# Performance work log

Hardware: AMD Instinct MI355X
Metric: run time of the kernel (lower is better)

Reference implementation:

```python
import jax, jax.numpy as jnp
import numpy as np

N = 50000
E = 800000
IN_C, HID_C, OUT_C = 256, 128, 64


def setup_inputs() -> dict:
    key = jax.random.key(0)
    k1, k2, k3, k4 = jax.random.split(key, 4)
    x = jax.random.normal(k1, (N, IN_C), dtype=jnp.float32)
    edge_index = jax.random.randint(k2, (2, E), 0, N, dtype=jnp.int64)
    # Glorot-ish init for GCN weights, zero bias (PyG default)
    W1 = jax.random.normal(k3, (IN_C, HID_C), dtype=jnp.float32) / np.sqrt(IN_C)
    b1 = jnp.zeros((HID_C,), dtype=jnp.float32)
    W2 = jax.random.normal(k4, (HID_C, OUT_C), dtype=jnp.float32) / np.sqrt(HID_C)
    b2 = jnp.zeros((OUT_C,), dtype=jnp.float32)
    return {"x": x, "edge_index": edge_index, "W1": W1, "b1": b1, "W2": W2, "b2": b2}


def _gcn_norm(edge_index, num_nodes):
    # Add self-loops, compute symmetric normalization D^-1/2 A D^-1/2 (PyG GCNConv default)
    loops = jnp.arange(num_nodes, dtype=edge_index.dtype)
    src = jnp.concatenate([edge_index[0], loops])  # message sources
    dst = jnp.concatenate([edge_index[1], loops])  # aggregation targets
    deg = jax.ops.segment_sum(jnp.ones_like(dst, dtype=jnp.float32), dst,
                              num_segments=num_nodes)
    dinv = jnp.where(deg > 0, jax.lax.rsqrt(deg), 0.0)
    norm = dinv[src] * dinv[dst]  # [E+N]
    return src, dst, norm


def _gcn_conv(x, W, b, src, dst, norm, num_nodes):
    h = x @ W                                   # [N, out]
    msg = h[src] * norm[:, None]                # gather + scale, [E+N, out]
    out = jax.ops.segment_sum(msg, dst, num_segments=num_nodes)  # scatter-add
    return out + b


def reference(x, edge_index, W1, b1, W2, b2):
    num_nodes = x.shape[0]
    src, dst, norm = _gcn_norm(edge_index, num_nodes)
    h = _gcn_conv(x, W1, b1, src, dst, norm, num_nodes)
    h = jax.nn.relu(h)
    # F.dropout(training=False) -> identity at inference
    return _gcn_conv(h, W2, b2, src, dst, norm, num_nodes)
```

## Files before the change

### kernel.cpp

```cpp
#include <hip/hip_runtime.h>
#include <hip/hip_bf16.h>


typedef __attribute__((ext_vector_type(8))) short short8;
typedef __attribute__((ext_vector_type(4))) float f32x4;

union BF8 {
    short8 s;
    uint4 u;
    __hip_bfloat162 h[4];
};

__device__ __forceinline__ unsigned short f32_to_bf16_rne(float f) {
    unsigned u = __float_as_uint(f);
    return (unsigned short)((u + 0x7fffu + ((u >> 16) & 1u)) >> 16);
}
__device__ __forceinline__ float bf_lo(unsigned v) { return __uint_as_float(v << 16); }
__device__ __forceinline__ float bf_hi(unsigned v) { return __uint_as_float(v & 0xffff0000u); }

#define ACHUNK 2048
#define BSH 6
#define BN 64
#define CAP 2048
#define EPT (CAP / 256)

__global__ void wfrag_zero_kernel(const float* __restrict__ W1, const float* __restrict__ W2,
                                  unsigned short* __restrict__ w1f,
                                  unsigned short* __restrict__ w2f,
                                  int* __restrict__ counts, int* __restrict__ bcursor,
                                  int n, int nbk) {
    int i = blockIdx.x * blockDim.x + threadIdx.x;
    if (i < n) counts[i] = 0;
    if (i < nbk) bcursor[i] = 0;
    const float* W;
    unsigned short* WF;
    int KS, NCOL, idx;
    if (i < 32768) {
        W = W1; WF = w1f; KS = 8; NCOL = 128; idx = i;
    } else if (i < 32768 + 8192) {
        W = W2; WF = w2f; KS = 4; NCOL = 64; idx = i - 32768;
    } else return;
    int j = idx & 7;
    int lane = (idx >> 3) & 63;
    int f = idx >> 9;
    int ks = f % KS, nt = f / KS;
    int m16 = lane & 15, quad = lane >> 4;
    int ncol = nt * 16 + m16;
    int k = ks * 32 + quad * 8 + j;
    WF[idx] = f32_to_bf16_rne(W[k * NCOL + ncol]);
}

__global__ __launch_bounds__(256) void gemm1_bucket_kernel(
    const float* __restrict__ A, const unsigned short* __restrict__ BFRAG,
    unsigned short* __restrict__ C, int M, int gGemm,
    const int* __restrict__ src, const int* __restrict__ dst,
    int* __restrict__ counts, int* __restrict__ bcursor,
    int2* __restrict__ tmp, int e, int nbk) {
    constexpr int NT = 8, KS = 8;
    constexpr int K = KS * 32;
    constexpr int LSTRIDE = K + 8;
    __shared__ char smem[64 * LSTRIDE * 2];

    const int tid = threadIdx.x;
    if ((int)blockIdx.x < gGemm) {
        unsigned short* Alds = (unsigned short*)smem;
        const int wave = tid >> 6, lane = tid & 63;
        const int quad = lane >> 4, m16 = lane & 15;
        const int rowBase = blockIdx.x * 64;

        constexpr int HALVES = K / 128;
#pragma unroll
        for (int h = 0; h < HALVES; h++) {
            f32x4 v[8];
#pragma unroll
            for (int it = 0; it < 8; it++) {
                int p = (h * 8 + it) * 1024 + tid * 4;
                int rg = rowBase + p / K;
                if (rg >= M) rg = M - 1;
                v[it] = *(const f32x4*)(A + (size_t)rg * K + (p % K));
            }
#pragma unroll
            for (int it = 0; it < 8; it++) {
                int p = (h * 8 + it) * 1024 + tid * 4;
                BF8 cv;
                cv.h[0] = __float22bfloat162_rn(make_float2(v[it].x, v[it].y));
                cv.h[1] = __float22bfloat162_rn(make_float2(v[it].z, v[it].w));
                *(uint2*)&Alds[(p / K) * LSTRIDE + (p % K)] = make_uint2(cv.u.x, cv.u.y);
            }
        }
        __syncthreads();

        const unsigned short* Afrag0 = &Alds[(wave * 16 + m16) * LSTRIDE + quad * 8];
        const uint4* Bfrag = (const uint4*)BFRAG + lane;

        f32x4 acc[NT];
#pragma unroll
        for (int nt = 0; nt < NT; nt++) acc[nt] = f32x4{0.f, 0.f, 0.f, 0.f};
#pragma unroll
        for (int ks = 0; ks < KS; ks++) {
            BF8 af;
            af.u = *(const uint4*)(Afrag0 + ks * 32);
#pragma unroll
            for (int nt = 0; nt < NT; nt++) {
                BF8 bf;
                bf.u = Bfrag[(nt * KS + ks) * 64];
                acc[nt] = __builtin_amdgcn_mfma_f32_16x16x32_bf16(af.s, bf.s, acc[nt], 0, 0, 0);
            }
        }
        const int rowOut = rowBase + wave * 16 + quad * 4;
#pragma unroll
        for (int nt = 0; nt < NT; nt++) {
#pragma unroll
            for (int r = 0; r < 4; r++) {
                int row = rowOut + r;
                if (row < M)
                    C[(size_t)row * 128 + nt * 16 + m16] = f32_to_bf16_rne(acc[nt][r]);
            }
        }
    } else {
        int* sdst = (int*)smem;
        int* hist = (int*)(smem + ACHUNK * 4);
        const int b0 = blockIdx.x - gGemm;
        const int start = b0 * ACHUNK;
        const int cnt = min(ACHUNK, e - start);
        for (int t = tid; t < nbk; t += 256) hist[t] = 0;
        __syncthreads();
        for (int i = tid; i < cnt; i += 256) {
            int d = dst[start + i];
            sdst[i] = d;
            atomicAdd(&counts[d], 1);
            atomicAdd(&hist[d >> BSH], 1);
        }
        __syncthreads();
        for (int t = tid; t < nbk; t += 256) {
            int h = hist[t];
            hist[t] = (h > 0) ? atomicAdd(&bcursor[t], h) : 0;
        }
        __syncthreads();
        for (int i = tid; i < cnt; i += 256) {
            int d = sdst[i];
            int slot = atomicAdd(&hist[d >> BSH], 1);
            if (slot < CAP)
                tmp[(size_t)(d >> BSH) * CAP + slot] = make_int2(src[start + i], d);
        }
    }
}

__global__ __launch_bounds__(256) void aggsort_gemm2_kernel(
    const int* __restrict__ counts, const int2* __restrict__ tmp,
    const int* __restrict__ bcursor,
    const unsigned short* __restrict__ hb,
    const float* __restrict__ bias1,
    const unsigned short* __restrict__ w2frag,
    int2* __restrict__ sedge, int2* __restrict__ nodeRange,
    unsigned short* __restrict__ h2, int n) {
    constexpr int LSTRIDE = 136;
    __shared__ int ecnt[BN];
    __shared__ int estart[BN];
    __shared__ int lcur[BN];
    __shared__ float ndinv[BN];
    __shared__ int ssrc[CAP];
    __shared__ float swt[CAP];
    __shared__ unsigned short a1lds[BN * LSTRIDE];

    const int tid = threadIdx.x;
    const int b = blockIdx.x;
    const int nodeBase = b << BSH;
    const int nNodes = min(BN, n - nodeBase);
    const int cnt = min(bcursor[b], CAP);

    if (tid < BN) ecnt[tid] = 0;
    __syncthreads();

    int2 er[EPT];
#pragma unroll
    for (int j = 0; j < EPT; j++) {
        int i = tid + j * 256;
        if (i < cnt) {
            int2 r = tmp[(size_t)b * CAP + i];
            er[j] = r;
            atomicAdd(&ecnt[r.y - nodeBase], 1);
        } else {
            er[j].x = -1;
            er[j].y = 0;
        }
    }
    __syncthreads();

    if (tid < BN) {
        int c = ecnt[tid];
        int x = c;
#pragma unroll
        for (int off = 1; off < 64; off <<= 1) {
            int y = __shfl_up(x, off, 64);
            if (tid >= off) x += y;
        }
        int st = x - c;
        estart[tid] = st;
        lcur[tid] = st;
        ndinv[tid] = (tid < nNodes) ? rsqrtf((float)counts[nodeBase + tid] + 1.0f) : 0.0f;
        if (tid < nNodes) nodeRange[nodeBase + tid] = make_int2(b * CAP + st, c);
    }
    __syncthreads();

#pragma unroll
    for (int j = 0; j < EPT; j++) {
        if (er[j].x >= 0) {
            int ln = er[j].y - nodeBase;
            float w = rsqrtf((float)counts[er[j].x] + 1.0f) * ndinv[ln];
            int pos = atomicAdd(&lcur[ln], 1);
            ssrc[pos] = er[j].x;
            swt[pos] = w;
            sedge[(size_t)b * CAP + pos] = make_int2(er[j].x, __float_as_int(w));
        }
    }
    __syncthreads();

    const int sub = tid & 15;
    const int qw = tid >> 4;
    for (int pass = 0; pass < BN / 16; pass++) {
        int ln = pass * 16 + qw;
        float a0 = 0.f, a1 = 0.f, a2 = 0.f, a3 = 0.f;
        float a4 = 0.f, a5 = 0.f, a6 = 0.f, a7 = 0.f;
        if (ln < nNodes) {
            int node = nodeBase + ln;
            float di = ndinv[ln];
            float d2 = di * di;
            uint4 sv = ((const uint4*)(hb + (size_t)node * 128))[sub];
            a0 = d2 * bf_lo(sv.x); a1 = d2 * bf_hi(sv.x);
            a2 = d2 * bf_lo(sv.y); a3 = d2 * bf_hi(sv.y);
            a4 = d2 * bf_lo(sv.z); a5 = d2 * bf_hi(sv.z);
            a6 = d2 * bf_lo(sv.w); a7 = d2 * bf_hi(sv.w);
            int beg = estart[ln];
            int end = beg + ecnt[ln];
            int i = beg;
            for (; i + 4 <= end; i += 4) {
                int s[4]; float w[4]; uint4 v[4];
#pragma unroll
                for (int j = 0; j < 4; j++) { s[j] = ssrc[i + j]; w[j] = swt[i + j]; }
#pragma unroll
                for (int j = 0; j < 4; j++)
                    v[j] = ((const uint4*)(hb + (size_t)s[j] * 128))[sub];
#pragma unroll
                for (int j = 0; j < 4; j++) {
                    a0 = fmaf(w[j], bf_lo(v[j].x), a0); a1 = fmaf(w[j], bf_hi(v[j].x), a1);
                    a2 = fmaf(w[j], bf_lo(v[j].y), a2); a3 = fmaf(w[j], bf_hi(v[j].y), a3);
                    a4 = fmaf(w[j], bf_lo(v[j].z), a4); a5 = fmaf(w[j], bf_hi(v[j].z), a5);
                    a6 = fmaf(w[j], bf_lo(v[j].w), a6); a7 = fmaf(w[j], bf_hi(v[j].w), a7);
                }
            }
            for (; i < end; ++i) {
                int s = ssrc[i];
                float w = swt[i];
                uint4 v = ((const uint4*)(hb + (size_t)s * 128))[sub];
                a0 = fmaf(w, bf_lo(v.x), a0); a1 = fmaf(w, bf_hi(v.x), a1);
                a2 = fmaf(w, bf_lo(v.y), a2); a3 = fmaf(w, bf_hi(v.y), a3);
                a4 = fmaf(w, bf_lo(v.z), a4); a5 = fmaf(w, bf_hi(v.z), a5);
                a6 = fmaf(w, bf_lo(v.w), a6); a7 = fmaf(w, bf_hi(v.w), a7);
            }
            float4 b0v = ((const float4*)bias1)[sub * 2];
            float4 b1v = ((const float4*)bias1)[sub * 2 + 1];
            a0 = fmaxf(a0 + b0v.x, 0.f); a1 = fmaxf(a1 + b0v.y, 0.f);
            a2 = fmaxf(a2 + b0v.z, 0.f); a3 = fmaxf(a3 + b0v.w, 0.f);
            a4 = fmaxf(a4 + b1v.x, 0.f); a5 = fmaxf(a5 + b1v.y, 0.f);
            a6 = fmaxf(a6 + b1v.z, 0.f); a7 = fmaxf(a7 + b1v.w, 0.f);
        }
        BF8 p;
        p.h[0] = __float22bfloat162_rn(make_float2(a0, a1));
        p.h[1] = __float22bfloat162_rn(make_float2(a2, a3));
        p.h[2] = __float22bfloat162_rn(make_float2(a4, a5));
        p.h[3] = __float22bfloat162_rn(make_float2(a6, a7));
        *(uint4*)&a1lds[ln * LSTRIDE + sub * 8] = p.u;
    }
    __syncthreads();

    const int wave = tid >> 6, lane = tid & 63;
    const int quad = lane >> 4, m16 = lane & 15;
    const unsigned short* Afrag0 = &a1lds[(wave * 16 + m16) * LSTRIDE + quad * 8];
    const uint4* Bfrag = (const uint4*)w2frag + lane;

    f32x4 acc[4];
#pragma unroll
    for (int nt = 0; nt < 4; nt++) acc[nt] = f32x4{0.f, 0.f, 0.f, 0.f};
#pragma unroll
    for (int ks = 0; ks < 4; ks++) {
        BF8 af;
        af.u = *(const uint4*)(Afrag0 + ks * 32);
#pragma unroll
        for (int nt = 0; nt < 4; nt++) {
            BF8 bf;
            bf.u = Bfrag[(nt * 4 + ks) * 64];
            acc[nt] = __builtin_amdgcn_mfma_f32_16x16x32_bf16(af.s, bf.s, acc[nt], 0, 0, 0);
        }
    }
    const int rowOut = wave * 16 + quad * 4;
#pragma unroll
    for (int nt = 0; nt < 4; nt++) {
#pragma unroll
        for (int r = 0; r < 4; r++) {
            int row = rowOut + r;
            if (row < nNodes)
                h2[(size_t)(nodeBase + row) * 64 + nt * 16 + m16] =
                    f32_to_bf16_rne(acc[nt][r]);
        }
    }
}

__global__ __launch_bounds__(256) void agg64_kernel(
    const int2* __restrict__ nodeRange, const int2* __restrict__ sedge,
    const unsigned short* __restrict__ hb, const int* __restrict__ counts,
    const float* __restrict__ bias, float* __restrict__ out, int n) {
    int node = blockIdx.x * 16 + (threadIdx.x >> 4);
    if (node >= n) return;
    int sub = threadIdx.x & 15;
    float di = rsqrtf((float)counts[node] + 1.0f);
    float d2 = di * di;
    uint2 sv = ((const uint2*)(hb + (size_t)node * 64))[sub];
    float a0 = d2 * bf_lo(sv.x), a1 = d2 * bf_hi(sv.x);
    float a2 = d2 * bf_lo(sv.y), a3 = d2 * bf_hi(sv.y);
    int2 nr = nodeRange[node];
    int beg = nr.x, end = nr.x + nr.y;
    int i = beg;
    for (; i + 8 <= end; i += 8) {
        int2 e[8];
        uint2 v[8];
#pragma unroll
        for (int j = 0; j < 8; j++) e[j] = sedge[i + j];
#pragma unroll
        for (int j = 0; j < 8; j++)
            v[j] = ((const uint2*)(hb + (size_t)e[j].x * 64))[sub];
#pragma unroll
        for (int j = 0; j < 8; j++) {
            float w = __int_as_float(e[j].y);
            a0 = fmaf(w, bf_lo(v[j].x), a0); a1 = fmaf(w, bf_hi(v[j].x), a1);
            a2 = fmaf(w, bf_lo(v[j].y), a2); a3 = fmaf(w, bf_hi(v[j].y), a3);
        }
    }
    for (; i + 4 <= end; i += 4) {
        int2 e[4];
        uint2 v[4];
#pragma unroll
        for (int j = 0; j < 4; j++) e[j] = sedge[i + j];
#pragma unroll
        for (int j = 0; j < 4; j++)
            v[j] = ((const uint2*)(hb + (size_t)e[j].x * 64))[sub];
#pragma unroll
        for (int j = 0; j < 4; j++) {
            float w = __int_as_float(e[j].y);
            a0 = fmaf(w, bf_lo(v[j].x), a0); a1 = fmaf(w, bf_hi(v[j].x), a1);
            a2 = fmaf(w, bf_lo(v[j].y), a2); a3 = fmaf(w, bf_hi(v[j].y), a3);
        }
    }
    for (; i < end; ++i) {
        int2 e = sedge[i];
        float w = __int_as_float(e.y);
        uint2 v = ((const uint2*)(hb + (size_t)e.x * 64))[sub];
        a0 = fmaf(w, bf_lo(v.x), a0); a1 = fmaf(w, bf_hi(v.x), a1);
        a2 = fmaf(w, bf_lo(v.y), a2); a3 = fmaf(w, bf_hi(v.y), a3);
    }
    float4 bv = ((const float4*)bias)[sub];
    ((float4*)(out + (size_t)node * 64))[sub] =
        make_float4(a0 + bv.x, a1 + bv.y, a2 + bv.z, a3 + bv.w);
}

extern "C" void kernel_launch(void* const* d_in, const int* in_sizes, int n_in,
                              void* d_out, int out_size, void* d_ws, size_t ws_size,
                              hipStream_t stream) {
    const float* x  = (const float*)d_in[0];
    const int*   ei = (const int*)d_in[1];
    const float* W1 = (const float*)d_in[2];
    const float* b1 = (const float*)d_in[3];
    const float* W2 = (const float*)d_in[4];
    const float* b2 = (const float*)d_in[5];
    float* out = (float*)d_out;

    const int IN_C = 256;
    const int N = in_sizes[0] / IN_C;
    const int E = in_sizes[1] / 2;
    const int* srcA = ei;
    const int* dstA = ei + E;

    char* ws = (char*)d_ws;
    const size_t KB = 1024, MB = 1024 * 1024;
    int*            counts    = (int*)(ws);
    int*            bcursor   = (int*)(ws + 256 * KB);
    unsigned short* w1f       = (unsigned short*)(ws + 1 * MB);
    unsigned short* w2f       = (unsigned short*)(ws + 1 * MB + 64 * KB);
    int2*           tmp       = (int2*)(ws + 2 * MB);
    int2*           sedge     = (int2*)(ws + 16 * MB);
    int2*           nodeRange = (int2*)(ws + 30 * MB);
    unsigned short* h1b       = (unsigned short*)(ws + 31 * MB);
    unsigned short* h2b       = (unsigned short*)(ws + 44 * MB);

    const int NB = (N + BN - 1) / BN;
    const int gGemm = (N + 63) / 64;
    const int nbA = (E + ACHUNK - 1) / ACHUNK;
    const int gWfrag = (max(N, 32768 + 8192) + 255) / 256;

    wfrag_zero_kernel<<<gWfrag, 256, 0, stream>>>(W1, W2, w1f, w2f, counts, bcursor, N, NB);
    gemm1_bucket_kernel<<<gGemm + nbA, 256, 0, stream>>>(
        x, w1f, h1b, N, gGemm, srcA, dstA, counts, bcursor, tmp, E, NB);
    aggsort_gemm2_kernel<<<NB, 256, 0, stream>>>(
        counts, tmp, bcursor, h1b, b1, w2f, sedge, nodeRange, h2b, N);
    agg64_kernel<<<(N + 15) / 16, 256, 0, stream>>>(nodeRange, sedge, h2b, counts, b2, out, N);
}
```

Before: 202.1 us.

## Shrink LDS footprints, add occupancy hints, and reorder bucket blocks first

The layer-1 GEMM now stages A in two K-halves of 128 columns, which halves its LDS tile, and the edge-bucketing blocks are scheduled before the GEMM blocks. The aggregation kernel drops its shared ssrc/swt staging and reads the sorted edge list from global memory. All three kernels get launch_bounds(256,8). Degree normalisation is computed from the local count instead of loading from the global counts array. Together these aim to raise occupancy and cut redundant loads, at the cost of an extra barrier in the GEMM and global re-reads of edges that likely hit cache.

```diff
diff --git a/kernel.cpp b/kernel.cpp
--- a/kernel.cpp
+++ b/kernel.cpp
@@ -50,61 +50,65 @@
     WF[idx] = f32_to_bf16_rne(W[k * NCOL + ncol]);
 }
 
-__global__ __launch_bounds__(256) void gemm1_bucket_kernel(
+__global__ __launch_bounds__(256, 8) void gemm1_bucket_kernel(
     const float* __restrict__ A, const unsigned short* __restrict__ BFRAG,
-    unsigned short* __restrict__ C, int M, int gGemm,
+    unsigned short* __restrict__ C, int M, int nbA,
     const int* __restrict__ src, const int* __restrict__ dst,
     int* __restrict__ counts, int* __restrict__ bcursor,
     int2* __restrict__ tmp, int e, int nbk) {
     constexpr int NT = 8, KS = 8;
     constexpr int K = KS * 32;
-    constexpr int LSTRIDE = K + 8;
-    __shared__ char smem[64 * LSTRIDE * 2];
+    constexpr int LSTRIDE = 136;
+    __shared__ unsigned short Alds[64 * LSTRIDE];
 
     const int tid = threadIdx.x;
-    if ((int)blockIdx.x < gGemm) {
-        unsigned short* Alds = (unsigned short*)smem;
+    if ((int)blockIdx.x >= nbA) {
         const int wave = tid >> 6, lane = tid & 63;
         const int quad = lane >> 4, m16 = lane & 15;
-        const int rowBase = blockIdx.x * 64;
-
-        constexpr int HALVES = K / 128;
-#pragma unroll
-        for (int h = 0; h < HALVES; h++) {
-            f32x4 v[8];
-#pragma unroll
-            for (int it = 0; it < 8; it++) {
-                int p = (h * 8 + it) * 1024 + tid * 4;
-                int rg = rowBase + p / K;
-                if (rg >= M) rg = M - 1;
-                v[it] = *(const f32x4*)(A + (size_t)rg * K + (p % K));
+        const int rowBase = (blockIdx.x - nbA) * 64;
+        const uint4* Bfrag = (const uint4*)BFRAG + lane;
+
+        f32x4 acc[NT];
+#pragma unroll
+        for (int nt = 0; nt < NT; nt++) acc[nt] = f32x4{0.f, 0.f, 0.f, 0.f};
+
+#pragma unroll
+        for (int h = 0; h < 2; h++) {
+            if (h) __syncthreads();
+#pragma unroll
+            for (int bt = 0; bt < 2; bt++) {
+                f32x4 v[4];
+#pragma unroll
+                for (int it = 0; it < 4; it++) {
+                    int p = (bt * 4 + it) * 1024 + tid * 4;
+                    int r = p >> 7, c = p & 127;
+                    int rg = rowBase + r;
+                    if (rg >= M) rg = M - 1;
+                    v[it] = *(const f32x4*)(A + (size_t)rg * K + h * 128 + c);
+                }
+#pragma unroll
+                for (int it = 0; it < 4; it++) {
+                    int p = (bt * 4 + it) * 1024 + tid * 4;
+                    int r = p >> 7, c = p & 127;
+                    BF8 cv;
+                    cv.h[0] = __float22bfloat162_rn(make_float2(v[it].x, v[it].y));
+                    cv.h[1] = __float22bfloat162_rn(make_float2(v[it].z, v[it].w));
+                    *(uint2*)&Alds[r * LSTRIDE + c] = make_uint2(cv.u.x, cv.u.y);
+                }
             }
-#pragma unroll
-            for (int it = 0; it < 8; it++) {
-                int p = (h * 8 + it) * 1024 + tid * 4;
-                BF8 cv;
-                cv.h[0] = __float22bfloat162_rn(make_float2(v[it].x, v[it].y));
-                cv.h[1] = __float22bfloat162_rn(make_float2(v[it].z, v[it].w));
-                *(uint2*)&Alds[(p / K) * LSTRIDE + (p % K)] = make_uint2(cv.u.x, cv.u.y);
-            }
-        }
-        __syncthreads();
-
-        const unsigned short* Afrag0 = &Alds[(wave * 16 + m16) * LSTRIDE + quad * 8];
-        const uint4* Bfrag = (const uint4*)BFRAG + lane;
-
-        f32x4 acc[NT];
-#pragma unroll
-        for (int nt = 0; nt < NT; nt++) acc[nt] = f32x4{0.f, 0.f, 0.f, 0.f};
-#pragma unroll
-        for (int ks = 0; ks < KS; ks++) {
-            BF8 af;
-            af.u = *(const uint4*)(Afrag0 + ks * 32);
-#pragma unroll
-            for (int nt = 0; nt < NT; nt++) {
-                BF8 bf;
-                bf.u = Bfrag[(nt * KS + ks) * 64];
-                acc[nt] = __builtin_amdgcn_mfma_f32_16x16x32_bf16(af.s, bf.s, acc[nt], 0, 0, 0);
+            __syncthreads();
+            const unsigned short* Afrag0 = &Alds[(wave * 16 + m16) * LSTRIDE + quad * 8];
+#pragma unroll
+            for (int ks = 0; ks < 4; ks++) {
+                BF8 af;
+                af.u = *(const uint4*)(Afrag0 + ks * 32);
+                int kg = h * 4 + ks;
+#pragma unroll
+                for (int nt = 0; nt < NT; nt++) {
+                    BF8 bf;
+                    bf.u = Bfrag[(nt * KS + kg) * 64];
+                    acc[nt] = __builtin_amdgcn_mfma_f32_16x16x32_bf16(af.s, bf.s, acc[nt], 0, 0, 0);
+                }
             }
         }
         const int rowOut = rowBase + wave * 16 + quad * 4;
@@ -118,9 +122,9 @@
             }
         }
     } else {
-        int* sdst = (int*)smem;
-        int* hist = (int*)(smem + ACHUNK * 4);
-        const int b0 = blockIdx.x - gGemm;
+        int* sdst = (int*)Alds;
+        int* hist = (int*)((char*)Alds + ACHUNK * 4);
+        const int b0 = blockIdx.x;
         const int start = b0 * ACHUNK;
         const int cnt = min(ACHUNK, e - start);
         for (int t = tid; t < nbk; t += 256) hist[t] = 0;
@@ -146,7 +150,7 @@
     }
 }
 
-__global__ __launch_bounds__(256) void aggsort_gemm2_kernel(
+__global__ __launch_bounds__(256, 8) void aggsort_gemm2_kernel(
     const int* __restrict__ counts, const int2* __restrict__ tmp,
     const int* __restrict__ bcursor,
     const unsigned short* __restrict__ hb,
@@ -159,8 +163,6 @@
     __shared__ int estart[BN];
     __shared__ int lcur[BN];
     __shared__ float ndinv[BN];
-    __shared__ int ssrc[CAP];
-    __shared__ float swt[CAP];
     __shared__ unsigned short a1lds[BN * LSTRIDE];
 
     const int tid = threadIdx.x;
@@ -198,7 +200,7 @@
         int st = x - c;
         estart[tid] = st;
         lcur[tid] = st;
-        ndinv[tid] = (tid < nNodes) ? rsqrtf((float)counts[nodeBase + tid] + 1.0f) : 0.0f;
+        ndinv[tid] = rsqrtf((float)c + 1.0f);
         if (tid < nNodes) nodeRange[nodeBase + tid] = make_int2(b * CAP + st, c);
     }
     __syncthreads();
@@ -209,8 +211,6 @@
             int ln = er[j].y - nodeBase;
             float w = rsqrtf((float)counts[er[j].x] + 1.0f) * ndinv[ln];
             int pos = atomicAdd(&lcur[ln], 1);
-            ssrc[pos] = er[j].x;
-            swt[pos] = w;
             sedge[(size_t)b * CAP + pos] = make_int2(er[j].x, __float_as_int(w));
         }
     }
@@ -231,28 +231,30 @@
             a2 = d2 * bf_lo(sv.y); a3 = d2 * bf_hi(sv.y);
             a4 = d2 * bf_lo(sv.z); a5 = d2 * bf_hi(sv.z);
             a6 = d2 * bf_lo(sv.w); a7 = d2 * bf_hi(sv.w);
+            const int2* seg = sedge + (size_t)b * CAP;
             int beg = estart[ln];
             int end = beg + ecnt[ln];
             int i = beg;
             for (; i + 4 <= end; i += 4) {
-                int s[4]; float w[4]; uint4 v[4];
-#pragma unroll
-                for (int j = 0; j < 4; j++) { s[j] = ssrc[i + j]; w[j] = swt[i + j]; }
+                int2 e[4]; uint4 v[4];
+#pragma unroll
+                for (int j = 0; j < 4; j++) e[j] = seg[i + j];
 #pragma unroll
                 for (int j = 0; j < 4; j++)
-                    v[j] = ((const uint4*)(hb + (size_t)s[j] * 128))[sub];
+                    v[j] = ((const uint4*)(hb + (size_t)e[j].x * 128))[sub];
 #pragma unroll
                 for (int j = 0; j < 4; j++) {
-                    a0 = fmaf(w[j], bf_lo(v[j].x), a0); a1 = fmaf(w[j], bf_hi(v[j].x), a1);
-                    a2 = fmaf(w[j], bf_lo(v[j].y), a2); a3 = fmaf(w[j], bf_hi(v[j].y), a3);
-                    a4 = fmaf(w[j], bf_lo(v[j].z), a4); a5 = fmaf(w[j], bf_hi(v[j].z), a5);
-                    a6 = fmaf(w[j], bf_lo(v[j].w), a6); a7 = fmaf(w[j], bf_hi(v[j].w), a7);
+                    float w = __int_as_float(e[j].y);
+                    a0 = fmaf(w, bf_lo(v[j].x), a0); a1 = fmaf(w, bf_hi(v[j].x), a1);
+                    a2 = fmaf(w, bf_lo(v[j].y), a2); a3 = fmaf(w, bf_hi(v[j].y), a3);
+                    a4 = fmaf(w, bf_lo(v[j].z), a4); a5 = fmaf(w, bf_hi(v[j].z), a5);
+                    a6 = fmaf(w, bf_lo(v[j].w), a6); a7 = fmaf(w, bf_hi(v[j].w), a7);
                 }
             }
             for (; i < end; ++i) {
-                int s = ssrc[i];
-                float w = swt[i];
-                uint4 v = ((const uint4*)(hb + (size_t)s * 128))[sub];
+                int2 e = seg[i];
+                float w = __int_as_float(e.y);
+                uint4 v = ((const uint4*)(hb + (size_t)e.x * 128))[sub];
                 a0 = fmaf(w, bf_lo(v.x), a0); a1 = fmaf(w, bf_hi(v.x), a1);
                 a2 = fmaf(w, bf_lo(v.y), a2); a3 = fmaf(w, bf_hi(v.y), a3);
                 a4 = fmaf(w, bf_lo(v.z), a4); a5 = fmaf(w, bf_hi(v.z), a5);
@@ -306,19 +308,19 @@
     }
 }
 
-__global__ __launch_bounds__(256) void agg64_kernel(
+__global__ __launch_bounds__(256, 8) void agg64_kernel(
     const int2* __restrict__ nodeRange, const int2* __restrict__ sedge,
-    const unsigned short* __restrict__ hb, const int* __restrict__ counts,
+    const unsigned short* __restrict__ hb,
     const float* __restrict__ bias, float* __restrict__ out, int n) {
     int node = blockIdx.x * 16 + (threadIdx.x >> 4);
     if (node >= n) return;
     int sub = threadIdx.x & 15;
-    float di = rsqrtf((float)counts[node] + 1.0f);
+    int2 nr = nodeRange[node];
+    float di = rsqrtf((float)nr.y + 1.0f);
     float d2 = di * di;
     uint2 sv = ((const uint2*)(hb + (size_t)node * 64))[sub];
     float a0 = d2 * bf_lo(sv.x), a1 = d2 * bf_hi(sv.x);
     float a2 = d2 * bf_lo(sv.y), a3 = d2 * bf_hi(sv.y);
-    int2 nr = nodeRange[node];
     int beg = nr.x, end = nr.x + nr.y;
     int i = beg;
     for (; i + 8 <= end; i += 8) {
@@ -398,9 +400,9 @@
     const int gWfrag = (max(N, 32768 + 8192) + 255) / 256;
 
     wfrag_zero_kernel<<<gWfrag, 256, 0, stream>>>(W1, W2, w1f, w2f, counts, bcursor, N, NB);
-    gemm1_bucket_kernel<<<gGemm + nbA, 256, 0, stream>>>(
-        x, w1f, h1b, N, gGemm, srcA, dstA, counts, bcursor, tmp, E, NB);
+    gemm1_bucket_kernel<<<nbA + gGemm, 256, 0, stream>>>(
+        x, w1f, h1b, N, nbA, srcA, dstA, counts, bcursor, tmp, E, NB);
     aggsort_gemm2_kernel<<<NB, 256, 0, stream>>>(
         counts, tmp, bcursor, h1b, b1, w2f, sedge, nodeRange, h2b, N);
-    agg64_kernel<<<(N + 15) / 16, 256, 0, stream>>>(nodeRange, sedge, h2b, counts, b2, out, N);
-}
+    agg64_kernel<<<(N + 15) / 16, 256, 0, stream>>>(nodeRange, sedge, h2b, b2, out, N);
+}
```

Measured after the change: 242.6 us. 20.0% more time.

## Split bucket cursors per XCD and derive degrees from local counts

Applied to the files above, without the earlier changes.

Bucket cursors and tmp slots are now partitioned per XCD (read from the hardware XCC_ID register), so the global atomics used while bucketing edges contend only within one die. The aggregation kernel loops over eight per-XCD sub-buckets instead of one contiguous bucket, computes the destination dinv from the local edge count, and gains an 8-wide gather unroll. agg64 reads the degree from nodeRange instead of counts and gets an occupancy hint in its launch bounds. Each per-XCD sub-bucket is capped at 256 edges, so skewed buckets could overflow and silently drop edges.

```diff
diff --git a/kernel.cpp b/kernel.cpp
--- a/kernel.cpp
+++ b/kernel.cpp
@@ -18,20 +18,27 @@
 __device__ __forceinline__ float bf_lo(unsigned v) { return __uint_as_float(v << 16); }
 __device__ __forceinline__ float bf_hi(unsigned v) { return __uint_as_float(v & 0xffff0000u); }
 
+__device__ __forceinline__ int xcc_id() {
+    int x;
+    asm volatile("s_getreg_b32 %0, hwreg(HW_REG_XCC_ID)" : "=s"(x));
+    return x & 7;
+}
+
 #define ACHUNK 2048
 #define BSH 6
 #define BN 64
 #define CAP 2048
-#define EPT (CAP / 256)
+#define CAPS 256
+#define NXCD 8
 
 __global__ void wfrag_zero_kernel(const float* __restrict__ W1, const float* __restrict__ W2,
                                   unsigned short* __restrict__ w1f,
                                   unsigned short* __restrict__ w2f,
                                   int* __restrict__ counts, int* __restrict__ bcursor,
-                                  int n, int nbk) {
+                                  int n, int nbk8) {
     int i = blockIdx.x * blockDim.x + threadIdx.x;
     if (i < n) counts[i] = 0;
-    if (i < nbk) bcursor[i] = 0;
+    if (i < nbk8) bcursor[i] = 0;
     const float* W;
     unsigned short* WF;
     int KS, NCOL, idx;
@@ -119,7 +126,8 @@
         }
     } else {
         int* sdst = (int*)smem;
-        int* hist = (int*)(smem + ACHUNK * 4);
+        int* hist = (int*)((char*)smem + ACHUNK * 4);
+        const int xcd = xcc_id();
         const int b0 = blockIdx.x - gGemm;
         const int start = b0 * ACHUNK;
         const int cnt = min(ACHUNK, e - start);
@@ -134,14 +142,15 @@
         __syncthreads();
         for (int t = tid; t < nbk; t += 256) {
             int h = hist[t];
-            hist[t] = (h > 0) ? atomicAdd(&bcursor[t], h) : 0;
+            hist[t] = (h > 0) ? atomicAdd(&bcursor[t * NXCD + xcd], h) : 0;
         }
         __syncthreads();
         for (int i = tid; i < cnt; i += 256) {
             int d = sdst[i];
             int slot = atomicAdd(&hist[d >> BSH], 1);
-            if (slot < CAP)
-                tmp[(size_t)(d >> BSH) * CAP + slot] = make_int2(src[start + i], d);
+            if (slot < CAPS)
+                tmp[((size_t)(d >> BSH) * NXCD + xcd) * CAPS + slot] =
+                    make_int2(src[start + i], d);
         }
     }
 }
@@ -167,23 +176,19 @@
     const int b = blockIdx.x;
     const int nodeBase = b << BSH;
     const int nNodes = min(BN, n - nodeBase);
-    const int cnt = min(bcursor[b], CAP);
+
+    int clen[NXCD];
+#pragma unroll
+    for (int xp = 0; xp < NXCD; xp++) clen[xp] = min(bcursor[b * NXCD + xp], CAPS);
 
     if (tid < BN) ecnt[tid] = 0;
     __syncthreads();
 
-    int2 er[EPT];
-#pragma unroll
-    for (int j = 0; j < EPT; j++) {
-        int i = tid + j * 256;
-        if (i < cnt) {
-            int2 r = tmp[(size_t)b * CAP + i];
-            er[j] = r;
-            atomicAdd(&ecnt[r.y - nodeBase], 1);
-        } else {
-            er[j].x = -1;
-            er[j].y = 0;
-        }
+#pragma unroll
+    for (int xp = 0; xp < NXCD; xp++) {
+        const int2* sp = tmp + ((size_t)b * NXCD + xp) * CAPS;
+        for (int i = tid; i < clen[xp]; i += 256)
+            atomicAdd(&ecnt[sp[i].y - nodeBase], 1);
     }
     __syncthreads();
 
@@ -198,20 +203,22 @@
         int st = x - c;
         estart[tid] = st;
         lcur[tid] = st;
-        ndinv[tid] = (tid < nNodes) ? rsqrtf((float)counts[nodeBase + tid] + 1.0f) : 0.0f;
+        ndinv[tid] = rsqrtf((float)c + 1.0f);
         if (tid < nNodes) nodeRange[nodeBase + tid] = make_int2(b * CAP + st, c);
     }
     __syncthreads();
 
 #pragma unroll
-    for (int j = 0; j < EPT; j++) {
-        if (er[j].x >= 0) {
-            int ln = er[j].y - nodeBase;
-            float w = rsqrtf((float)counts[er[j].x] + 1.0f) * ndinv[ln];
+    for (int xp = 0; xp < NXCD; xp++) {
+        const int2* sp = tmp + ((size_t)b * NXCD + xp) * CAPS;
+        for (int i = tid; i < clen[xp]; i += 256) {
+            int2 r = sp[i];
+            int ln = r.y - nodeBase;
+            float w = rsqrtf((float)counts[r.x] + 1.0f) * ndinv[ln];
             int pos = atomicAdd(&lcur[ln], 1);
-            ssrc[pos] = er[j].x;
+            ssrc[pos] = r.x;
             swt[pos] = w;
-            sedge[(size_t)b * CAP + pos] = make_int2(er[j].x, __float_as_int(w));
+            sedge[(size_t)b * CAP + pos] = make_int2(r.x, __float_as_int(w));
         }
     }
     __syncthreads();
@@ -234,6 +241,21 @@
             int beg = estart[ln];
             int end = beg + ecnt[ln];
             int i = beg;
+            for (; i + 8 <= end; i += 8) {
+                int s[8]; float w[8]; uint4 v[8];
+#pragma unroll
+                for (int j = 0; j < 8; j++) { s[j] = ssrc[i + j]; w[j] = swt[i + j]; }
+#pragma unroll
+                for (int j = 0; j < 8; j++)
+                    v[j] = ((const uint4*)(hb + (size_t)s[j] * 128))[sub];
+#pragma unroll
+                for (int j = 0; j < 8; j++) {
+                    a0 = fmaf(w[j], bf_lo(v[j].x), a0); a1 = fmaf(w[j], bf_hi(v[j].x), a1);
+                    a2 = fmaf(w[j], bf_lo(v[j].y), a2); a3 = fmaf(w[j], bf_hi(v[j].y), a3);
+                    a4 = fmaf(w[j], bf_lo(v[j].z), a4); a5 = fmaf(w[j], bf_hi(v[j].z), a5);
+                    a6 = fmaf(w[j], bf_lo(v[j].w), a6); a7 = fmaf(w[j], bf_hi(v[j].w), a7);
+                }
+            }
             for (; i + 4 <= end; i += 4) {
                 int s[4]; float w[4]; uint4 v[4];
 #pragma unroll
@@ -306,19 +328,19 @@
     }
 }
 
-__global__ __launch_bounds__(256) void agg64_kernel(
+__global__ __launch_bounds__(256, 8) void agg64_kernel(
     const int2* __restrict__ nodeRange, const int2* __restrict__ sedge,
-    const unsigned short* __restrict__ hb, const int* __restrict__ counts,
+    const unsigned short* __restrict__ hb,
     const float* __restrict__ bias, float* __restrict__ out, int n) {
     int node = blockIdx.x * 16 + (threadIdx.x >> 4);
     if (node >= n) return;
     int sub = threadIdx.x & 15;
-    float di = rsqrtf((float)counts[node] + 1.0f);
+    int2 nr = nodeRange[node];
+    float di = rsqrtf((float)nr.y + 1.0f);
     float d2 = di * di;
     uint2 sv = ((const uint2*)(hb + (size_t)node * 64))[sub];
     float a0 = d2 * bf_lo(sv.x), a1 = d2 * bf_hi(sv.x);
     float a2 = d2 * bf_lo(sv.y), a3 = d2 * bf_hi(sv.y);
-    int2 nr = nodeRange[node];
     int beg = nr.x, end = nr.x + nr.y;
     int i = beg;
     for (; i + 8 <= end; i += 8) {
@@ -397,10 +419,11 @@
     const int nbA = (E + ACHUNK - 1) / ACHUNK;
     const int gWfrag = (max(N, 32768 + 8192) + 255) / 256;
 
-    wfrag_zero_kernel<<<gWfrag, 256, 0, stream>>>(W1, W2, w1f, w2f, counts, bcursor, N, NB);
+    wfrag_zero_kernel<<<gWfrag, 256, 0, stream>>>(W1, W2, w1f, w2f, counts, bcursor,
+                                                  N, NB * NXCD);
     gemm1_bucket_kernel<<<gGemm + nbA, 256, 0, stream>>>(
         x, w1f, h1b, N, gGemm, srcA, dstA, counts, bcursor, tmp, E, NB);
     aggsort_gemm2_kernel<<<NB, 256, 0, stream>>>(
         counts, tmp, bcursor, h1b, b1, w2f, sedge, nodeRange, h2b, N);
-    agg64_kernel<<<(N + 15) / 16, 256, 0, stream>>>(nodeRange, sedge, h2b, counts, b2, out, N);
-}
+    agg64_kernel<<<(N + 15) / 16, 256, 0, stream>>>(nodeRange, sedge, h2b, b2, out, N);
+}
```

Measured after the change: 206.0 us. No clear change (+1.9%).

## Pre-convert x to bf16 in prep kernel and read GEMM1 A fragments directly

Applied to the files above, without the earlier changes.

Moves the fp32-to-bf16 conversion of x into the prep kernel and writes it to a workspace buffer. GEMM1 then loads A fragments straight from global memory instead of staging them through LDS, which shrinks its shared memory use and drops a barrier. The cost is an extra full write and read of x in bf16. The change also computes degree normalisation from values already loaded rather than re-reading counts, and adds an occupancy hint on the final aggregation kernel.

```diff
diff --git a/kernel.cpp b/kernel.cpp
--- a/kernel.cpp
+++ b/kernel.cpp
@@ -24,73 +24,66 @@
 #define CAP 2048
 #define EPT (CAP / 256)
 
-__global__ void wfrag_zero_kernel(const float* __restrict__ W1, const float* __restrict__ W2,
-                                  unsigned short* __restrict__ w1f,
-                                  unsigned short* __restrict__ w2f,
-                                  int* __restrict__ counts, int* __restrict__ bcursor,
-                                  int n, int nbk) {
+__global__ void prep_kernel(const float* __restrict__ x,
+                            const float* __restrict__ W1, const float* __restrict__ W2,
+                            unsigned short* __restrict__ xb,
+                            unsigned short* __restrict__ w1f,
+                            unsigned short* __restrict__ w2f,
+                            int* __restrict__ counts, int* __restrict__ bcursor,
+                            int n, int nbk, int nx8) {
     int i = blockIdx.x * blockDim.x + threadIdx.x;
-    if (i < n) counts[i] = 0;
-    if (i < nbk) bcursor[i] = 0;
+    if (i < nx8) {
+        f32x4 v0 = *(const f32x4*)(x + (size_t)i * 8);
+        f32x4 v1 = *(const f32x4*)(x + (size_t)i * 8 + 4);
+        BF8 cv;
+        cv.h[0] = __float22bfloat162_rn(make_float2(v0.x, v0.y));
+        cv.h[1] = __float22bfloat162_rn(make_float2(v0.z, v0.w));
+        cv.h[2] = __float22bfloat162_rn(make_float2(v1.x, v1.y));
+        cv.h[3] = __float22bfloat162_rn(make_float2(v1.z, v1.w));
+        *(uint4*)(xb + (size_t)i * 8) = cv.u;
+        return;
+    }
+    int j = i - nx8;
+    if (j < n) counts[j] = 0;
+    if (j < nbk) bcursor[j] = 0;
     const float* W;
     unsigned short* WF;
     int KS, NCOL, idx;
-    if (i < 32768) {
-        W = W1; WF = w1f; KS = 8; NCOL = 128; idx = i;
-    } else if (i < 32768 + 8192) {
-        W = W2; WF = w2f; KS = 4; NCOL = 64; idx = i - 32768;
+    if (j < 32768) {
+        W = W1; WF = w1f; KS = 8; NCOL = 128; idx = j;
+    } else if (j < 32768 + 8192) {
+        W = W2; WF = w2f; KS = 4; NCOL = 64; idx = j - 32768;
     } else return;
-    int j = idx & 7;
+    int jj = idx & 7;
     int lane = (idx >> 3) & 63;
     int f = idx >> 9;
     int ks = f % KS, nt = f / KS;
     int m16 = lane & 15, quad = lane >> 4;
     int ncol = nt * 16 + m16;
-    int k = ks * 32 + quad * 8 + j;
+    int k = ks * 32 + quad * 8 + jj;
     WF[idx] = f32_to_bf16_rne(W[k * NCOL + ncol]);
 }
 
 __global__ __launch_bounds__(256) void gemm1_bucket_kernel(
-    const float* __restrict__ A, const unsigned short* __restrict__ BFRAG,
+    const unsigned short* __restrict__ A,
+    const unsigned short* __restrict__ BFRAG,
     unsigned short* __restrict__ C, int M, int gGemm,
     const int* __restrict__ src, const int* __restrict__ dst,
     int* __restrict__ counts, int* __restrict__ bcursor,
     int2* __restrict__ tmp, int e, int nbk) {
     constexpr int NT = 8, KS = 8;
-    constexpr int K = KS * 32;
-    constexpr int LSTRIDE = K + 8;
-    __shared__ char smem[64 * LSTRIDE * 2];
+    __shared__ int sdst[ACHUNK];
+    __shared__ int hist[1024];
 
     const int tid = threadIdx.x;
     if ((int)blockIdx.x < gGemm) {
-        unsigned short* Alds = (unsigned short*)smem;
         const int wave = tid >> 6, lane = tid & 63;
         const int quad = lane >> 4, m16 = lane & 15;
         const int rowBase = blockIdx.x * 64;
 
-        constexpr int HALVES = K / 128;
-#pragma unroll
-        for (int h = 0; h < HALVES; h++) {
-            f32x4 v[8];
-#pragma unroll
-            for (int it = 0; it < 8; it++) {
-                int p = (h * 8 + it) * 1024 + tid * 4;
-                int rg = rowBase + p / K;
-                if (rg >= M) rg = M - 1;
-                v[it] = *(const f32x4*)(A + (size_t)rg * K + (p % K));
-            }
-#pragma unroll
-            for (int it = 0; it < 8; it++) {
-                int p = (h * 8 + it) * 1024 + tid * 4;
-                BF8 cv;
-                cv.h[0] = __float22bfloat162_rn(make_float2(v[it].x, v[it].y));
-                cv.h[1] = __float22bfloat162_rn(make_float2(v[it].z, v[it].w));
-                *(uint2*)&Alds[(p / K) * LSTRIDE + (p % K)] = make_uint2(cv.u.x, cv.u.y);
-            }
-        }
-        __syncthreads();
-
-        const unsigned short* Afrag0 = &Alds[(wave * 16 + m16) * LSTRIDE + quad * 8];
+        int rg = rowBase + wave * 16 + m16;
+        if (rg >= M) rg = M - 1;
+        const unsigned short* Arow = A + (size_t)rg * 256 + quad * 8;
         const uint4* Bfrag = (const uint4*)BFRAG + lane;
 
         f32x4 acc[NT];
@@ -99,7 +92,7 @@
 #pragma unroll
         for (int ks = 0; ks < KS; ks++) {
             BF8 af;
-            af.u = *(const uint4*)(Afrag0 + ks * 32);
+            af.u = *(const uint4*)(Arow + ks * 32);
 #pragma unroll
             for (int nt = 0; nt < NT; nt++) {
                 BF8 bf;
@@ -118,8 +111,6 @@
             }
         }
     } else {
-        int* sdst = (int*)smem;
-        int* hist = (int*)(smem + ACHUNK * 4);
         const int b0 = blockIdx.x - gGemm;
         const int start = b0 * ACHUNK;
         const int cnt = min(ACHUNK, e - start);
@@ -140,7 +131,7 @@
         for (int i = tid; i < cnt; i += 256) {
             int d = sdst[i];
             int slot = atomicAdd(&hist[d >> BSH], 1);
-            if (slot < CAP)
+            if ((unsigned)slot < (unsigned)CAP)
                 tmp[(size_t)(d >> BSH) * CAP + slot] = make_int2(src[start + i], d);
         }
     }
@@ -198,7 +189,7 @@
         int st = x - c;
         estart[tid] = st;
         lcur[tid] = st;
-        ndinv[tid] = (tid < nNodes) ? rsqrtf((float)counts[nodeBase + tid] + 1.0f) : 0.0f;
+        ndinv[tid] = rsqrtf((float)c + 1.0f);
         if (tid < nNodes) nodeRange[nodeBase + tid] = make_int2(b * CAP + st, c);
     }
     __syncthreads();
@@ -306,19 +297,19 @@
     }
 }
 
-__global__ __launch_bounds__(256) void agg64_kernel(
+__global__ __launch_bounds__(256, 8) void agg64_kernel(
     const int2* __restrict__ nodeRange, const int2* __restrict__ sedge,
-    const unsigned short* __restrict__ hb, const int* __restrict__ counts,
+    const unsigned short* __restrict__ hb,
     const float* __restrict__ bias, float* __restrict__ out, int n) {
     int node = blockIdx.x * 16 + (threadIdx.x >> 4);
     if (node >= n) return;
     int sub = threadIdx.x & 15;
-    float di = rsqrtf((float)counts[node] + 1.0f);
+    int2 nr = nodeRange[node];
+    float di = rsqrtf((float)nr.y + 1.0f);
     float d2 = di * di;
     uint2 sv = ((const uint2*)(hb + (size_t)node * 64))[sub];
     float a0 = d2 * bf_lo(sv.x), a1 = d2 * bf_hi(sv.x);
     float a2 = d2 * bf_lo(sv.y), a3 = d2 * bf_hi(sv.y);
-    int2 nr = nodeRange[node];
     int beg = nr.x, end = nr.x + nr.y;
     int i = beg;
     for (; i + 8 <= end; i += 8) {
@@ -391,16 +382,20 @@
     int2*           nodeRange = (int2*)(ws + 30 * MB);
     unsigned short* h1b       = (unsigned short*)(ws + 31 * MB);
     unsigned short* h2b       = (unsigned short*)(ws + 44 * MB);
+    unsigned short* xb        = (unsigned short*)(ws + 52 * MB);
 
     const int NB = (N + BN - 1) / BN;
     const int gGemm = (N + 63) / 64;
     const int nbA = (E + ACHUNK - 1) / ACHUNK;
-    const int gWfrag = (max(N, 32768 + 8192) + 255) / 256;
-
-    wfrag_zero_kernel<<<gWfrag, 256, 0, stream>>>(W1, W2, w1f, w2f, counts, bcursor, N, NB);
+    const int nx8 = N * 32;
+    const int tailT = max(N, 32768 + 8192);
+    const int gPrep = (nx8 + tailT + 255) / 256;
+
+    prep_kernel<<<gPrep, 256, 0, stream>>>(x, W1, W2, xb, w1f, w2f, counts, bcursor,
+                                           N, NB, nx8);
     gemm1_bucket_kernel<<<gGemm + nbA, 256, 0, stream>>>(
-        x, w1f, h1b, N, gGemm, srcA, dstA, counts, bcursor, tmp, E, NB);
+        xb, w1f, h1b, N, gGemm, srcA, dstA, counts, bcursor, tmp, E, NB);
     aggsort_gemm2_kernel<<<NB, 256, 0, stream>>>(
         counts, tmp, bcursor, h1b, b1, w2f, sedge, nodeRange, h2b, N);
-    agg64_kernel<<<(N + 15) / 16, 256, 0, stream>>>(nodeRange, sedge, h2b, counts, b2, out, N);
-}
+    agg64_kernel<<<(N + 15) / 16, 256, 0, stream>>>(nodeRange, sedge, h2b, b2, out, N);
+}
```

Result: slower. 212.3 us (+5.1%).
